# Optimization experiments

Hardware: AMD Instinct MI355X
Metric: run time of the kernel (lower is better)

## Reference

```python
import jax, jax.numpy as jnp
import numpy as np

S, A, B, D = 4, 64, 2048, 384
H1, H2, H3 = 128, 128, 64


def setup_inputs() -> dict:
    key = jax.random.key(0)
    ks = jax.random.split(key, 6)
    x = jax.random.normal(ks[0], (B, A, D), dtype=jnp.float32)
    species = jax.random.randint(ks[1], (A,), 0, S, dtype=jnp.int32)
    # per-species stacked MLP weights, scaled ~1/sqrt(fan_in) like reset_parameters
    W0 = jax.random.normal(ks[2], (S, D, H1), dtype=jnp.float32) / np.sqrt(D)
    W1 = jax.random.normal(ks[3], (S, H1, H2), dtype=jnp.float32) / np.sqrt(H1)
    W2 = jax.random.normal(ks[4], (S, H2, H3), dtype=jnp.float32) / np.sqrt(H2)
    W3 = jax.random.normal(ks[5], (S, H3, 1), dtype=jnp.float32) / np.sqrt(H3)
    b0 = jnp.zeros((S, H1), jnp.float32)
    b1 = jnp.zeros((S, H2), jnp.float32)
    b2 = jnp.zeros((S, H3), jnp.float32)
    b3 = jnp.zeros((S, 1), jnp.float32)
    return {"x": x, "species": species, "W0": W0, "b0": b0, "W1": W1,
            "b1": b1, "W2": W2, "b2": b2, "W3": W3, "b3": b3}


def reference(x, species, W0, b0, W1, b1, W2, b2, W3, b3):
    # Gather per-atom species weights once, then batched per-atom GEMMs.
    # x: [B, A, D]; species: [A]
    y = jnp.einsum('bad,adh->bah', x, W0[species]) + b0[species]
    y = jnp.exp(-y * y)
    y = jnp.einsum('bah,ahk->bak', y, W1[species]) + b1[species]
    y = jnp.exp(-y * y)
    y = jnp.einsum('bak,akm->bam', y, W2[species]) + b2[species]
    y = jnp.exp(-y * y)
    y = jnp.einsum('bam,amo->bao', y, W3[species]) + b3[species]  # [B, A, 1]
    return jnp.squeeze(jnp.sum(y, axis=1))  # [B]
```

## Files before the change

kernel.cpp:

```cpp
#include <hip/hip_runtime.h>

#define S_DIM 4
#define A_DIM 64
#define B_DIM 2048
#define D_DIM 384
#define H1D 128
#define H2D 128
#define H3D 64
#define MT 64

typedef __attribute__((ext_vector_type(8))) short short8;
typedef __attribute__((ext_vector_type(4))) float float4v;

__device__ __forceinline__ unsigned short f2bf(float f) {
  unsigned u = __float_as_uint(f);
  u += 0x7FFFu + ((u >> 16) & 1u);
  return (unsigned short)(u >> 16);
}

__global__ __launch_bounds__(256) void prep_weights(
    const float* __restrict__ W0, const float* __restrict__ W1,
    const float* __restrict__ W2,
    unsigned short* __restrict__ W0T, unsigned short* __restrict__ W1T,
    unsigned short* __restrict__ W2T) {
  __shared__ float tile[32][33];
  int b = blockIdx.x;
  const float* src; unsigned short* dst; int R, C, dt, ht, s;
  if (b < 192) {
    s = b / 48; int t = b % 48; dt = t / 4; ht = t % 4;
    src = W0 + s * D_DIM * H1D; dst = W0T + s * H1D * D_DIM; R = D_DIM; C = H1D;
  } else if (b < 256) {
    int bb = b - 192; s = bb / 16; int t = bb % 16; dt = t / 4; ht = t % 4;
    src = W1 + s * H1D * H2D; dst = W1T + s * H2D * H1D; R = H1D; C = H2D;
  } else {
    int bb = b - 256; s = bb / 8; int t = bb % 8; dt = t / 2; ht = t % 2;
    src = W2 + s * H2D * H3D; dst = W2T + s * H3D * H2D; R = H2D; C = H3D;
  }
  int tx = threadIdx.x & 31, ty = threadIdx.x >> 5;
#pragma unroll
  for (int k = 0; k < 4; ++k)
    tile[ty + 8 * k][tx] = src[(size_t)(dt * 32 + ty + 8 * k) * C + ht * 32 + tx];
  __syncthreads();
#pragma unroll
  for (int k = 0; k < 4; ++k)
    dst[(size_t)(ht * 32 + ty + 8 * k) * R + dt * 32 + tx] = f2bf(tile[tx][ty + 8 * k]);
}

__global__ __launch_bounds__(256, 3) void mlp_fused(
    const float* __restrict__ x, const int* __restrict__ species,
    const unsigned short* __restrict__ W0T, const unsigned short* __restrict__ W1T,
    const unsigned short* __restrict__ W2T,
    const float* __restrict__ b0, const float* __restrict__ b1,
    const float* __restrict__ b2, const float* __restrict__ W3,
    const float* __restrict__ b3, float* __restrict__ out) {
  __shared__ __align__(16) unsigned short xsH1[MT][136];
  __shared__ __align__(16) unsigned short H0s[MT][136];
  __shared__ float H2s[MT][69];
  __shared__ float W3s[H3D];

  const int a = blockIdx.y;
  const int brow0 = blockIdx.x * MT;
  const int sp = species[a];
  const int tid = threadIdx.x;
  const int wave = tid >> 6;
  const int lane = tid & 63;
  const int q = lane >> 4;
  const int r = lane & 15;

  if (tid < H3D) W3s[tid] = W3[sp * H3D + tid];

  const float4v zero = {0.f, 0.f, 0.f, 0.f};

  const int srow = tid >> 2;
  const int c4 = tid & 3;
  const float* xrow = x + ((size_t)(brow0 + srow) * A_DIM + a) * D_DIM;

  float4v acc0[4][2];
#pragma unroll
  for (int g = 0; g < 4; ++g) { acc0[g][0] = zero; acc0[g][1] = zero; }
  const unsigned short* w0base = W0T + (size_t)sp * H1D * D_DIM + (wave * 32 + r) * D_DIM + q * 8;

#pragma unroll
  for (int st = 0; st < 3; ++st) {
    const int ks = st * 128;
    short8 bf[4][2];
#pragma unroll
    for (int kk = 0; kk < 4; ++kk)
#pragma unroll
      for (int n = 0; n < 2; ++n)
        bf[kk][n] = *(const short8*)(w0base + n * 16 * D_DIM + ks + kk * 32);
    float4v xv[8];
#pragma unroll
    for (int j = 0; j < 8; ++j)
      xv[j] = *(const float4v*)(xrow + ks + c4 * 4 + j * 16);
    __syncthreads();
#pragma unroll
    for (int j = 0; j < 8; ++j) {
      unsigned short* p = &xsH1[srow][c4 * 4 + j * 16];
      p[0] = f2bf(xv[j][0]); p[1] = f2bf(xv[j][1]);
      p[2] = f2bf(xv[j][2]); p[3] = f2bf(xv[j][3]);
    }
    __syncthreads();
#pragma unroll
    for (int g = 0; g < 4; ++g)
#pragma unroll
      for (int kk = 0; kk < 4; ++kk) {
        short8 af = *(const short8*)&xsH1[g * 16 + r][kk * 32 + q * 8];
        acc0[g][0] = __builtin_amdgcn_mfma_f32_16x16x32_bf16(af, bf[kk][0], acc0[g][0], 0, 0, 0);
        acc0[g][1] = __builtin_amdgcn_mfma_f32_16x16x32_bf16(af, bf[kk][1], acc0[g][1], 0, 0, 0);
      }
  }
  __syncthreads();
  {
    const float* b0p = b0 + sp * H1D;
#pragma unroll
    for (int n = 0; n < 2; ++n) {
      float bias = b0p[wave * 32 + n * 16 + r];
#pragma unroll
      for (int g = 0; g < 4; ++g)
#pragma unroll
        for (int i = 0; i < 4; ++i) {
          float y = acc0[g][n][i] + bias;
          H0s[g * 16 + q * 4 + i][wave * 32 + n * 16 + r] = f2bf(__expf(-y * y));
        }
    }
  }
  __syncthreads();

  float4v acc1[4][2];
#pragma unroll
  for (int g = 0; g < 4; ++g) { acc1[g][0] = zero; acc1[g][1] = zero; }
  {
    const unsigned short* w1base = W1T + (size_t)sp * H2D * H1D + (wave * 32 + r) * H1D + q * 8;
    short8 bf[4][2];
#pragma unroll
    for (int kk = 0; kk < 4; ++kk)
#pragma unroll
      for (int n = 0; n < 2; ++n)
        bf[kk][n] = *(const short8*)(w1base + n * 16 * H1D + kk * 32);
#pragma unroll
    for (int g = 0; g < 4; ++g)
#pragma unroll
      for (int kk = 0; kk < 4; ++kk) {
        short8 af = *(const short8*)&H0s[g * 16 + r][kk * 32 + q * 8];
        acc1[g][0] = __builtin_amdgcn_mfma_f32_16x16x32_bf16(af, bf[kk][0], acc1[g][0], 0, 0, 0);
        acc1[g][1] = __builtin_amdgcn_mfma_f32_16x16x32_bf16(af, bf[kk][1], acc1[g][1], 0, 0, 0);
      }
    const float* b1p = b1 + sp * H2D;
#pragma unroll
    for (int n = 0; n < 2; ++n) {
      float bias = b1p[wave * 32 + n * 16 + r];
#pragma unroll
      for (int g = 0; g < 4; ++g)
#pragma unroll
        for (int i = 0; i < 4; ++i) {
          float y = acc1[g][n][i] + bias;
          xsH1[g * 16 + q * 4 + i][wave * 32 + n * 16 + r] = f2bf(__expf(-y * y));
        }
    }
  }
  __syncthreads();

  {
    float4v acc2[4];
#pragma unroll
    for (int g = 0; g < 4; ++g) acc2[g] = zero;
    const unsigned short* w2base = W2T + (size_t)sp * H3D * H2D + (wave * 16 + r) * H2D + q * 8;
    short8 bf[4];
#pragma unroll
    for (int kk = 0; kk < 4; ++kk)
      bf[kk] = *(const short8*)(w2base + kk * 32);
#pragma unroll
    for (int g = 0; g < 4; ++g)
#pragma unroll
      for (int kk = 0; kk < 4; ++kk) {
        short8 af = *(const short8*)&xsH1[g * 16 + r][kk * 32 + q * 8];
        acc2[g] = __builtin_amdgcn_mfma_f32_16x16x32_bf16(af, bf[kk], acc2[g], 0, 0, 0);
      }
    float bias = b2[sp * H3D + wave * 16 + r];
#pragma unroll
    for (int g = 0; g < 4; ++g)
#pragma unroll
      for (int i = 0; i < 4; ++i) {
        float y = acc2[g][i] + bias;
        H2s[g * 16 + q * 4 + i][wave * 16 + r] = __expf(-y * y);
      }
  }
  __syncthreads();

  {
    const int row = tid >> 2;
    const int seg = tid & 3;
    float s = 0.f;
#pragma unroll
    for (int j = 0; j < 16; ++j)
      s += H2s[row][seg * 16 + j] * W3s[seg * 16 + j];
    s += __shfl_xor(s, 1);
    s += __shfl_xor(s, 2);
    if (seg == 0) atomicAdd(&out[brow0 + row], s + b3[sp]);
  }
}

extern "C" void kernel_launch(void* const* d_in, const int* in_sizes, int n_in,
                              void* d_out, int out_size, void* d_ws, size_t ws_size,
                              hipStream_t stream) {
  const float* x       = (const float*)d_in[0];
  const int*   species = (const int*)d_in[1];
  const float* W0 = (const float*)d_in[2];
  const float* b0 = (const float*)d_in[3];
  const float* W1 = (const float*)d_in[4];
  const float* b1 = (const float*)d_in[5];
  const float* W2 = (const float*)d_in[6];
  const float* b2 = (const float*)d_in[7];
  const float* W3 = (const float*)d_in[8];
  const float* b3 = (const float*)d_in[9];
  float* out = (float*)d_out;

  unsigned short* W0T = (unsigned short*)d_ws;
  unsigned short* W1T = W0T + S_DIM * H1D * D_DIM;
  unsigned short* W2T = W1T + S_DIM * H2D * H1D;

  hipMemsetAsync(d_out, 0, out_size * sizeof(float), stream);
  prep_weights<<<dim3(288), dim3(256), 0, stream>>>(W0, W1, W2, W0T, W1T, W2T);
  mlp_fused<<<dim3(B_DIM / MT, A_DIM), dim3(256), 0, stream>>>(
      x, species, W0T, W1T, W2T, b0, b1, b2, W3, b3, out);
}
```

Measured before the change: 310.6 us.

## Stage full x row tile into LDS upfront with aliased buffers and vector stores

Loads the whole 64x384 x tile into shared memory in one staged pass, interleaving global loads with bf16 conversion, instead of three k-steps each bracketed by two barriers. LDS buffers are aliased (x, H0, H1, H2 share one region) to keep the footprint near occupancy-3 limits. Bf16 stores are packed into 8-byte writes and the final dot product uses float4 LDS reads. This removes per-step barriers and exposes more memory-level parallelism, at the cost of higher register pressure from holding two 8-vector x batches plus weight fragments.

```diff
diff --git a/kernel.cpp b/kernel.cpp
--- a/kernel.cpp
+++ b/kernel.cpp
@@ -16,6 +16,13 @@
   unsigned u = __float_as_uint(f);
   u += 0x7FFFu + ((u >> 16) & 1u);
   return (unsigned short)(u >> 16);
+}
+
+__device__ __forceinline__ void store_bf4(unsigned short* p, float4v v) {
+  union { unsigned short s[4]; uint2 u; } t;
+  t.s[0] = f2bf(v[0]); t.s[1] = f2bf(v[1]);
+  t.s[2] = f2bf(v[2]); t.s[3] = f2bf(v[3]);
+  *(uint2*)p = t.u;
 }
 
 __global__ __launch_bounds__(256) void prep_weights(
@@ -53,10 +60,13 @@
     const float* __restrict__ b0, const float* __restrict__ b1,
     const float* __restrict__ b2, const float* __restrict__ W3,
     const float* __restrict__ b3, float* __restrict__ out) {
-  __shared__ __align__(16) unsigned short xsH1[MT][136];
-  __shared__ __align__(16) unsigned short H0s[MT][136];
-  __shared__ float H2s[MT][69];
-  __shared__ float W3s[H3D];
+  __shared__ __align__(16) unsigned short bufA[MT * 392];
+  __shared__ __align__(16) float W3s[H3D];
+
+  unsigned short* xs = bufA;
+  unsigned short* H0 = bufA;
+  unsigned short* H1 = bufA + MT * 136;
+  float* H2 = (float*)bufA;
 
   const int a = blockIdx.y;
   const int brow0 = blockIdx.x * MT;
@@ -73,41 +83,56 @@
 
   const int srow = tid >> 2;
   const int c4 = tid & 3;
-  const float* xrow = x + ((size_t)(brow0 + srow) * A_DIM + a) * D_DIM;
+  const float* xrow = x + ((size_t)(brow0 + srow) * A_DIM + a) * D_DIM + c4 * 4;
+  unsigned short* xdst = xs + srow * 392 + c4 * 4;
+
+  const unsigned short* w0base =
+      W0T + (size_t)sp * H1D * D_DIM + (wave * 32 + r) * D_DIM + q * 8;
+
+  float4v xva[8], xvb[8];
+#pragma unroll
+  for (int j = 0; j < 8; ++j) xva[j] = *(const float4v*)(xrow + j * 16);
+#pragma unroll
+  for (int j = 0; j < 8; ++j) xvb[j] = *(const float4v*)(xrow + (j + 8) * 16);
+  short8 bf0[4][2];
+#pragma unroll
+  for (int kk = 0; kk < 4; ++kk)
+#pragma unroll
+    for (int n = 0; n < 2; ++n)
+      bf0[kk][n] = *(const short8*)(w0base + n * 16 * D_DIM + kk * 32);
+#pragma unroll
+  for (int j = 0; j < 8; ++j) store_bf4(xdst + j * 16, xva[j]);
+#pragma unroll
+  for (int j = 0; j < 8; ++j) xva[j] = *(const float4v*)(xrow + (j + 16) * 16);
+#pragma unroll
+  for (int j = 0; j < 8; ++j) store_bf4(xdst + (j + 8) * 16, xvb[j]);
+#pragma unroll
+  for (int j = 0; j < 8; ++j) store_bf4(xdst + (j + 16) * 16, xva[j]);
+  __syncthreads();
 
   float4v acc0[4][2];
 #pragma unroll
   for (int g = 0; g < 4; ++g) { acc0[g][0] = zero; acc0[g][1] = zero; }
-  const unsigned short* w0base = W0T + (size_t)sp * H1D * D_DIM + (wave * 32 + r) * D_DIM + q * 8;
-
 #pragma unroll
   for (int st = 0; st < 3; ++st) {
-    const int ks = st * 128;
-    short8 bf[4][2];
-#pragma unroll
-    for (int kk = 0; kk < 4; ++kk)
-#pragma unroll
-      for (int n = 0; n < 2; ++n)
-        bf[kk][n] = *(const short8*)(w0base + n * 16 * D_DIM + ks + kk * 32);
-    float4v xv[8];
-#pragma unroll
-    for (int j = 0; j < 8; ++j)
-      xv[j] = *(const float4v*)(xrow + ks + c4 * 4 + j * 16);
-    __syncthreads();
-#pragma unroll
-    for (int j = 0; j < 8; ++j) {
-      unsigned short* p = &xsH1[srow][c4 * 4 + j * 16];
-      p[0] = f2bf(xv[j][0]); p[1] = f2bf(xv[j][1]);
-      p[2] = f2bf(xv[j][2]); p[3] = f2bf(xv[j][3]);
+    short8 bfs[4][2];
+    if (st == 0) {
+#pragma unroll
+      for (int kk = 0; kk < 4; ++kk) { bfs[kk][0] = bf0[kk][0]; bfs[kk][1] = bf0[kk][1]; }
+    } else {
+#pragma unroll
+      for (int kk = 0; kk < 4; ++kk)
+#pragma unroll
+        for (int n = 0; n < 2; ++n)
+          bfs[kk][n] = *(const short8*)(w0base + n * 16 * D_DIM + st * 128 + kk * 32);
     }
-    __syncthreads();
 #pragma unroll
     for (int g = 0; g < 4; ++g)
 #pragma unroll
       for (int kk = 0; kk < 4; ++kk) {
-        short8 af = *(const short8*)&xsH1[g * 16 + r][kk * 32 + q * 8];
-        acc0[g][0] = __builtin_amdgcn_mfma_f32_16x16x32_bf16(af, bf[kk][0], acc0[g][0], 0, 0, 0);
-        acc0[g][1] = __builtin_amdgcn_mfma_f32_16x16x32_bf16(af, bf[kk][1], acc0[g][1], 0, 0, 0);
+        short8 af = *(const short8*)(xs + (g * 16 + r) * 392 + st * 128 + kk * 32 + q * 8);
+        acc0[g][0] = __builtin_amdgcn_mfma_f32_16x16x32_bf16(af, bfs[kk][0], acc0[g][0], 0, 0, 0);
+        acc0[g][1] = __builtin_amdgcn_mfma_f32_16x16x32_bf16(af, bfs[kk][1], acc0[g][1], 0, 0, 0);
       }
   }
   __syncthreads();
@@ -121,17 +146,18 @@
 #pragma unroll
         for (int i = 0; i < 4; ++i) {
           float y = acc0[g][n][i] + bias;
-          H0s[g * 16 + q * 4 + i][wave * 32 + n * 16 + r] = f2bf(__expf(-y * y));
+          H0[(g * 16 + q * 4 + i) * 136 + wave * 32 + n * 16 + r] = f2bf(__expf(-y * y));
         }
     }
   }
   __syncthreads();
 
-  float4v acc1[4][2];
-#pragma unroll
-  for (int g = 0; g < 4; ++g) { acc1[g][0] = zero; acc1[g][1] = zero; }
-  {
-    const unsigned short* w1base = W1T + (size_t)sp * H2D * H1D + (wave * 32 + r) * H1D + q * 8;
+  {
+    float4v acc1[4][2];
+#pragma unroll
+    for (int g = 0; g < 4; ++g) { acc1[g][0] = zero; acc1[g][1] = zero; }
+    const unsigned short* w1base =
+        W1T + (size_t)sp * H2D * H1D + (wave * 32 + r) * H1D + q * 8;
     short8 bf[4][2];
 #pragma unroll
     for (int kk = 0; kk < 4; ++kk)
@@ -142,7 +168,7 @@
     for (int g = 0; g < 4; ++g)
 #pragma unroll
       for (int kk = 0; kk < 4; ++kk) {
-        short8 af = *(const short8*)&H0s[g * 16 + r][kk * 32 + q * 8];
+        short8 af = *(const short8*)(H0 + (g * 16 + r) * 136 + kk * 32 + q * 8);
         acc1[g][0] = __builtin_amdgcn_mfma_f32_16x16x32_bf16(af, bf[kk][0], acc1[g][0], 0, 0, 0);
         acc1[g][1] = __builtin_amdgcn_mfma_f32_16x16x32_bf16(af, bf[kk][1], acc1[g][1], 0, 0, 0);
       }
@@ -155,7 +181,7 @@
 #pragma unroll
         for (int i = 0; i < 4; ++i) {
           float y = acc1[g][n][i] + bias;
-          xsH1[g * 16 + q * 4 + i][wave * 32 + n * 16 + r] = f2bf(__expf(-y * y));
+          H1[(g * 16 + q * 4 + i) * 136 + wave * 32 + n * 16 + r] = f2bf(__expf(-y * y));
         }
     }
   }
@@ -165,7 +191,8 @@
     float4v acc2[4];
 #pragma unroll
     for (int g = 0; g < 4; ++g) acc2[g] = zero;
-    const unsigned short* w2base = W2T + (size_t)sp * H3D * H2D + (wave * 16 + r) * H2D + q * 8;
+    const unsigned short* w2base =
+        W2T + (size_t)sp * H3D * H2D + (wave * 16 + r) * H2D + q * 8;
     short8 bf[4];
 #pragma unroll
     for (int kk = 0; kk < 4; ++kk)
@@ -174,7 +201,7 @@
     for (int g = 0; g < 4; ++g)
 #pragma unroll
       for (int kk = 0; kk < 4; ++kk) {
-        short8 af = *(const short8*)&xsH1[g * 16 + r][kk * 32 + q * 8];
+        short8 af = *(const short8*)(H1 + (g * 16 + r) * 136 + kk * 32 + q * 8);
         acc2[g] = __builtin_amdgcn_mfma_f32_16x16x32_bf16(af, bf[kk], acc2[g], 0, 0, 0);
       }
     float bias = b2[sp * H3D + wave * 16 + r];
@@ -183,7 +210,7 @@
 #pragma unroll
       for (int i = 0; i < 4; ++i) {
         float y = acc2[g][i] + bias;
-        H2s[g * 16 + q * 4 + i][wave * 16 + r] = __expf(-y * y);
+        H2[(g * 16 + q * 4 + i) * 68 + wave * 16 + r] = __expf(-y * y);
       }
   }
   __syncthreads();
@@ -191,10 +218,12 @@
   {
     const int row = tid >> 2;
     const int seg = tid & 3;
-    float s = 0.f;
-#pragma unroll
-    for (int j = 0; j < 16; ++j)
-      s += H2s[row][seg * 16 + j] * W3s[seg * 16 + j];
+    const float4v* h2p = (const float4v*)(H2 + row * 68 + seg * 16);
+    const float4v* w3p = (const float4v*)(W3s + seg * 16);
+    float4v sv = zero;
+#pragma unroll
+    for (int jj = 0; jj < 4; ++jj) sv += h2p[jj] * w3p[jj];
+    float s = sv[0] + sv[1] + sv[2] + sv[3];
     s += __shfl_xor(s, 1);
     s += __shfl_xor(s, 2);
     if (seg == 0) atomicAdd(&out[brow0 + row], s + b3[sp]);
```

Measured after the change: 318.5 us. +2.6%, slower.
